# Kernel optimization log

Measured on AMD Instinct MI355X. Metric: run time of the kernel, lower is better.

## Reference

```python
import jax, jax.numpy as jnp
import numpy as np

B, NQ, NK, DQ, DK, DV, H = 4, 512, 512, 512, 512, 512, 128
NEG_INF = -1e20


def setup_inputs() -> dict:
    key = jax.random.key(0)
    ks = jax.random.split(key, 7)
    Q = jax.random.normal(ks[0], (B, NQ, DQ), dtype=jnp.float32)
    K = jax.random.normal(ks[1], (B, NK, DK), dtype=jnp.float32)
    V = jax.random.normal(ks[2], (B, NK, DV), dtype=jnp.float32)
    # learned params (LazyLinear, bias=False): y = x @ W with W[in, out]
    Wq = jax.random.normal(ks[3], (DQ, H), dtype=jnp.float32) / np.sqrt(DQ)
    Wk = jax.random.normal(ks[4], (DK, H), dtype=jnp.float32) / np.sqrt(DK)
    wv = jax.random.normal(ks[5], (H,), dtype=jnp.float32) / np.sqrt(H)
    valid_lens = jax.random.randint(ks[6], (B,), 1, NK + 1).astype(jnp.int64)
    return {"Q": Q, "K": K, "V": V, "Wq": Wq, "Wk": Wk, "wv": wv,
            "valid_lens": valid_lens}


def reference(Q, K, V, Wq, Wk, wv, valid_lens):
    # Project queries and keys to shared hidden size H
    Qp = Q @ Wq                      # (B, NQ, H)
    Kp = K @ Wk                      # (B, NK, H)
    # Additive (Bahdanau) broadcast: (B, NQ, NK, H)
    S = jnp.tanh(Qp[:, :, None, :] + Kp[:, None, :, :])
    # Linear score to scalar: (B, NQ, NK)
    scores = jnp.einsum('bqkh,h->bqk', S, wv)
    # Mask positions k >= valid_lens[b] (1-D valid_lens broadcast over queries)
    kv_idx = jnp.arange(scores.shape[-1])[None, None, :]
    mask = kv_idx < valid_lens[:, None, None]
    scores = jnp.where(mask, scores, NEG_INF)
    W = jax.nn.softmax(scores, axis=-1)  # dropout rate 0.0 -> identity
    return jnp.einsum('bqk,bkv->bqv', W, V)
```

## Files before the change

kernel.cpp:

```cpp
#include <hip/hip_runtime.h>

#define B_   4
#define NQ_  512
#define NK_  512
#define D_   512
#define H_   128

typedef __attribute__((ext_vector_type(8))) short short8;
typedef __attribute__((ext_vector_type(8))) unsigned short ushort8;
typedef __attribute__((ext_vector_type(4))) float f32x4;

__device__ __forceinline__ float fexp2(float x) { return __builtin_amdgcn_exp2f(x); }
__device__ __forceinline__ float frcp(float x)  { return __builtin_amdgcn_rcpf(x); }
__device__ __forceinline__ unsigned short f2bf(float f) {
    unsigned int u = __builtin_bit_cast(unsigned int, f);
    u += 0x7FFFu + ((u >> 16) & 1u);
    return (unsigned short)(u >> 16);
}
__device__ __forceinline__ float bf2f(unsigned short h) {
    return __builtin_bit_cast(float, (unsigned int)h << 16);
}


#define WS_EQK   0
#define WS_WP    524288
#define WS_WBF   524544
#define WS_VT    1048832
#define WS_WTHI  1573120
#define WS_WTLO  1638656

__global__ __launch_bounds__(256) void prep_kernel(
    const float* __restrict__ V, const float* __restrict__ Wq,
    const float* __restrict__ Wk, const float* __restrict__ wv,
    const int* __restrict__ valid_lens,
    float* __restrict__ wp, unsigned short* __restrict__ Vt,
    unsigned short* __restrict__ WThi, unsigned short* __restrict__ WTlo)
{
    __shared__ __align__(16) float smem[64 * 69];
    const int t = threadIdx.x;

    if (blockIdx.x < 256) {
        const int id = blockIdx.x;
        const int kt = id & 7, dt = (id >> 3) & 7, b = id >> 6;
        const int vl = valid_lens[b];

        if (kt * 64 >= ((vl + 127) & ~127)) return;

        if (kt * 64 >= vl) {
            #pragma unroll
            for (int p = 0; p < 4; ++p) {
                const int idx = p * 256 + t;
                const int d  = idx >> 4;
                const int k4 = (idx & 15) * 4;
                ushort4 z; z.x = 0; z.y = 0; z.z = 0; z.w = 0;
                *reinterpret_cast<ushort4*>(
                    Vt + ((size_t)b * D_ + dt * 64 + d) * NK_ + kt * 64 + k4) = z;
            }
            return;
        }

        float (*Vl)[69] = (float(*)[69])smem;

        #pragma unroll
        for (int p = 0; p < 4; ++p) {
            const int idx = p * 256 + t;
            const int r  = idx >> 4;
            const int c4 = (idx & 15) * 4;
            const float4 v = *reinterpret_cast<const float4*>(
                V + ((size_t)b * NK_ + kt * 64 + r) * D_ + dt * 64 + c4);
            Vl[r][c4 + 0] = v.x; Vl[r][c4 + 1] = v.y;
            Vl[r][c4 + 2] = v.z; Vl[r][c4 + 3] = v.w;
        }
        __syncthreads();

        #pragma unroll
        for (int p = 0; p < 4; ++p) {
            const int idx = p * 256 + t;
            const int d  = idx >> 4;
            const int k4 = (idx & 15) * 4;
            ushort4 o;
            o.x = f2bf(Vl[k4 + 0][d]); o.y = f2bf(Vl[k4 + 1][d]);
            o.z = f2bf(Vl[k4 + 2][d]); o.w = f2bf(Vl[k4 + 3][d]);
            *reinterpret_cast<ushort4*>(
                Vt + ((size_t)b * D_ + dt * 64 + d) * NK_ + kt * 64 + k4) = o;
        }
    } else {
        if (blockIdx.x == 256 && t < 64) {
            const float2 w2 = reinterpret_cast<const float2*>(wv)[t];
            const float wn0 = -2.0f * w2.x;
            const float wn1 = -2.0f * w2.y;
            reinterpret_cast<float4*>(wp)[t] =
                make_float4(wn0, wn1, wn0 + wn1, 0.0f);
        }
        const int wid  = blockIdx.x - 256;
        const int mat  = wid >> 4;
        const int tile = wid & 15;
        const int kt   = tile >> 1;
        const int ct   = tile & 1;
        const float* __restrict__ Wm = mat ? Wk : Wq;
        float (*Wl)[69] = (float(*)[69])smem;

        #pragma unroll
        for (int p = 0; p < 4; ++p) {
            const int idx = p * 256 + t;
            const int r  = idx >> 4;
            const int c4 = (idx & 15) * 4;
            const float4 v = *reinterpret_cast<const float4*>(
                Wm + (size_t)(kt * 64 + r) * H_ + ct * 64 + c4);
            Wl[r][c4 + 0] = v.x; Wl[r][c4 + 1] = v.y;
            Wl[r][c4 + 2] = v.z; Wl[r][c4 + 3] = v.w;
        }
        __syncthreads();

        const int c  = t >> 2;
        const int kq = (t & 3) * 16;
        ushort8 ph0, pl0, ph1, pl1;
        #pragma unroll
        for (int j = 0; j < 8; ++j) {
            const float x = Wl[kq + j][c];
            const unsigned short h = f2bf(x);
            ph0[j] = h; pl0[j] = f2bf(x - bf2f(h));
        }
        #pragma unroll
        for (int j = 0; j < 8; ++j) {
            const float x = Wl[kq + 8 + j][c];
            const unsigned short h = f2bf(x);
            ph1[j] = h; pl1[j] = f2bf(x - bf2f(h));
        }
        const size_t off =
            ((size_t)(mat * H_ + ct * 64 + c)) * 512 + kt * 64 + kq;
        *reinterpret_cast<ushort8*>(WThi + off)     = ph0;
        *reinterpret_cast<ushort8*>(WThi + off + 8) = ph1;
        *reinterpret_cast<ushort8*>(WTlo + off)     = pl0;
        *reinterpret_cast<ushort8*>(WTlo + off + 8) = pl1;
    }
}

__global__ __launch_bounds__(512, 2) void proj_kernel(
    const float* __restrict__ Q, const float* __restrict__ K,
    const unsigned short* __restrict__ WThi,
    const unsigned short* __restrict__ WTlo,
    const int* __restrict__ valid_lens,
    float* __restrict__ Eqk)
{
    __shared__ __align__(16) unsigned short Ahi[16][520];
    __shared__ __align__(16) unsigned short Alo[16][520];
    const int t  = threadIdx.x;
    const int r0 = blockIdx.x * 16;
    const bool isQ = r0 < 2048;
    const float* __restrict__ X = isQ ? Q : K;
    const int xr0    = isQ ? r0 : r0 - 2048;
    const int matoff = isQ ? 0 : (H_ * 512);

    if (!isQ) {
        const int kr = xr0 & 511;
        const int bb = xr0 >> 9;
        if (kr >= valid_lens[bb]) return;
    }

    #pragma unroll
    for (int p = 0; p < 4; ++p) {
        const int idx = p * 512 + t;
        const int row = idx >> 7;
        const int kq  = (idx & 127) * 4;
        const float4 v = *reinterpret_cast<const float4*>(
            X + (size_t)(xr0 + row) * D_ + kq);
        ushort4 h, l;
        h.x = f2bf(v.x); l.x = f2bf(v.x - bf2f(h.x));
        h.y = f2bf(v.y); l.y = f2bf(v.y - bf2f(h.y));
        h.z = f2bf(v.z); l.z = f2bf(v.z - bf2f(h.z));
        h.w = f2bf(v.w); l.w = f2bf(v.w - bf2f(h.w));
        *reinterpret_cast<ushort4*>(&Ahi[row][kq]) = h;
        *reinterpret_cast<ushort4*>(&Alo[row][kq]) = l;
    }
    __syncthreads();

    const int wave = __builtin_amdgcn_readfirstlane(t >> 6);
    const int lane = t & 63;
    const int m    = lane & 15;
    const int quad = lane >> 4;

    const unsigned short* __restrict__ Bh =
        WThi + matoff + ((size_t)(wave * 16 + m)) * 512 + quad * 8;
    const unsigned short* __restrict__ Bl =
        WTlo + matoff + ((size_t)(wave * 16 + m)) * 512 + quad * 8;

    f32x4 accA = {0.f, 0.f, 0.f, 0.f};
    f32x4 accB = {0.f, 0.f, 0.f, 0.f};
    #pragma unroll
    for (int ksg = 0; ksg < 16; ++ksg) {
        const int kk = ksg * 32;
        const short8 bh = *reinterpret_cast<const short8*>(Bh + kk);
        const short8 bl = *reinterpret_cast<const short8*>(Bl + kk);
        const short8 ah = *reinterpret_cast<const short8*>(&Ahi[m][kk + quad * 8]);
        const short8 al = *reinterpret_cast<const short8*>(&Alo[m][kk + quad * 8]);
        f32x4& acc = (ksg & 1) ? accB : accA;
        acc = __builtin_amdgcn_mfma_f32_16x16x32_bf16(ah, bh, acc, 0, 0, 0);
        acc = __builtin_amdgcn_mfma_f32_16x16x32_bf16(al, bh, acc, 0, 0, 0);
        acc = __builtin_amdgcn_mfma_f32_16x16x32_bf16(ah, bl, acc, 0, 0, 0);
    }

    const float C2 = 2.88539008177792681472f;
    const int col = wave * 16 + m;
    #pragma unroll
    for (int i = 0; i < 4; ++i) {
        Eqk[(size_t)(r0 + quad * 4 + i) * H_ + col] =
            fexp2(C2 * (accA[i] + accB[i]));
    }
}

__global__ __launch_bounds__(512, 4) void score_softmax_kernel(
    const float* __restrict__ Eqk, const float* __restrict__ wp,
    const int* __restrict__ valid_lens, unsigned short* __restrict__ Wbf)
{
    const int rb   = blockIdx.x;
    const int t    = threadIdx.x;
    const int w    = __builtin_amdgcn_readfirstlane(t >> 6);
    const int lane = t & 63;
    const int rloc = w >> 1;
    const int half = w & 1;
    const int row  = rb * 4 + rloc;
    const int b    = row >> 9;

    __shared__ __align__(16) float4 Ks[2 * 64 * 33];
    __shared__ float redM[4][2], redS[4][2];

    const int vl = valid_lens[b];

    const float4* __restrict__ Q4 =
        reinterpret_cast<const float4*>(Eqk + (size_t)row * H_);
    const float4* __restrict__ wp4 = reinterpret_cast<const float4*>(wp);
    const float4* __restrict__ Kp4 =
        reinterpret_cast<const float4*>(Eqk + (size_t)(2048 + b * NK_) * H_);

    float vals[4];

    for (int c = 0; c < 4; ++c) {
        if (c) __syncthreads();
        #pragma unroll
        for (int p = 0; p < 8; ++p) {
            const int hh = p >> 2;
            if (hh * 256 + c * 64 < vl) {
                const int r  = (p & 3) * 16 + (t >> 5);
                const int h4 = t & 31;
                Ks[(hh * 64 + r) * 33 + h4] =
                    Kp4[(size_t)(hh * 256 + c * 64 + r) * 32 + h4];
            }
        }
        __syncthreads();

        float s = 0.0f;
        if (half * 256 + c * 64 < vl) {
            #pragma unroll 4
            for (int g = 0; g < 32; ++g) {
                const float4 kv = Ks[(half * 64 + lane) * 33 + g];
                const float4 qa = Q4[g];
                const float4 wa = wp4[2 * g];
                const float4 wb = wp4[2 * g + 1];
                const float e0 = qa.x * kv.x;
                const float e1 = qa.y * kv.y;
                const float e2 = qa.z * kv.z;
                const float e3 = qa.w * kv.w;
                const float D01 = 1.0f + fmaf(e0, e1, e0 + e1);
                const float D23 = 1.0f + fmaf(e2, e3, e2 + e3);
                const float n01 = fmaf(wa.y, e0, fmaf(wa.x, e1, wa.z));
                const float n23 = fmaf(wb.y, e2, fmaf(wb.x, e3, wb.z));
                const float N   = fmaf(n23, D01, n01 * D23);
                s = fmaf(N, frcp(D01 * D23), s);
            }
        }
        vals[c] = s;
    }

    const float L2E = 1.44269504088896340736f;
    float m = -1e30f;
    #pragma unroll
    for (int c = 0; c < 4; ++c) {
        const int k = half * 256 + c * 64 + lane;
        vals[c] = (k < vl) ? vals[c] : -1e30f;
        m = fmaxf(m, vals[c]);
    }
    #pragma unroll
    for (int off = 32; off >= 1; off >>= 1)
        m = fmaxf(m, __shfl_xor(m, off, 64));
    float sum = 0.0f;
    #pragma unroll
    for (int c = 0; c < 4; ++c)
        sum += fexp2((vals[c] - m) * L2E);
    #pragma unroll
    for (int off = 32; off >= 1; off >>= 1)
        sum += __shfl_xor(sum, off, 64);

    if (lane == 0) { redM[rloc][half] = m; redS[rloc][half] = sum; }
    __syncthreads();

    const float m0 = redM[rloc][0], m1 = redM[rloc][1];
    const float s0 = redS[rloc][0], s1 = redS[rloc][1];
    const float M  = fmaxf(m0, m1);
    const float S  = fmaf(s0, fexp2((m0 - M) * L2E),
                          s1 * fexp2((m1 - M) * L2E));
    const float inv = frcp(S);

    unsigned short* __restrict__ dst = Wbf + (size_t)row * NK_ + half * 256;
    #pragma unroll
    for (int c = 0; c < 4; ++c)
        dst[c * 64 + lane] = f2bf(fexp2((vals[c] - M) * L2E) * inv);
}

__global__ __launch_bounds__(256) void av_gemm_kernel(
    const unsigned short* __restrict__ Wbf, const unsigned short* __restrict__ Vt,
    const int* __restrict__ valid_lens, float* __restrict__ O)
{
    const int c0 = blockIdx.x * 64;
    const int r0 = blockIdx.y * 64;
    const int b  = blockIdx.z;
    const int t  = threadIdx.x;
    const int wave = __builtin_amdgcn_readfirstlane(t >> 6);
    const int lane = t & 63;
    const int m    = lane & 15;
    const int quad = lane >> 4;

    const int vl = valid_lens[b];

    __shared__ unsigned short Al [64][136];
    __shared__ unsigned short Btl[64][136];

    f32x4 acc0 = {0.f,0.f,0.f,0.f}, acc1 = {0.f,0.f,0.f,0.f};
    f32x4 acc2 = {0.f,0.f,0.f,0.f}, acc3 = {0.f,0.f,0.f,0.f};

    for (int kc = 0; kc < 4; ++kc) {
        if (kc * 128 >= vl) break;
        if (kc) __syncthreads();
        #pragma unroll
        for (int p = 0; p < 4; ++p) {
            const int idx = p * 256 + t;
            const int rl = idx >> 4;
            const int k8 = (idx & 15) * 8;
            *reinterpret_cast<uint4*>(&Al[rl][k8]) =
                *reinterpret_cast<const uint4*>(
                    Wbf + ((size_t)b * NQ_ + r0 + rl) * NK_ + kc * 128 + k8);
            *reinterpret_cast<uint4*>(&Btl[rl][k8]) =
                *reinterpret_cast<const uint4*>(
                    Vt + ((size_t)b * D_ + c0 + rl) * NK_ + kc * 128 + k8);
        }
        __syncthreads();

        #pragma unroll
        for (int sub = 0; sub < 4; ++sub) {
            const int kcol = sub * 32 + quad * 8;
            const short8 a = *reinterpret_cast<const short8*>(&Al[wave * 16 + m][kcol]);
            const short8 b0 = *reinterpret_cast<const short8*>(&Btl[ 0 + m][kcol]);
            const short8 b1 = *reinterpret_cast<const short8*>(&Btl[16 + m][kcol]);
            const short8 b2 = *reinterpret_cast<const short8*>(&Btl[32 + m][kcol]);
            const short8 b3 = *reinterpret_cast<const short8*>(&Btl[48 + m][kcol]);
            acc0 = __builtin_amdgcn_mfma_f32_16x16x32_bf16(a, b0, acc0, 0, 0, 0);
            acc1 = __builtin_amdgcn_mfma_f32_16x16x32_bf16(a, b1, acc1, 0, 0, 0);
            acc2 = __builtin_amdgcn_mfma_f32_16x16x32_bf16(a, b2, acc2, 0, 0, 0);
            acc3 = __builtin_amdgcn_mfma_f32_16x16x32_bf16(a, b3, acc3, 0, 0, 0);
        }
    }

    const size_t rowbase = (size_t)b * NQ_ + r0 + wave * 16 + quad * 4;
    #pragma unroll
    for (int i = 0; i < 4; ++i) {
        float* __restrict__ orow = O + (rowbase + i) * D_ + c0 + m;
        orow[ 0] = acc0[i];
        orow[16] = acc1[i];
        orow[32] = acc2[i];
        orow[48] = acc3[i];
    }
}

extern "C" void kernel_launch(void* const* d_in, const int* in_sizes, int n_in,
                              void* d_out, int out_size, void* d_ws, size_t ws_size,
                              hipStream_t stream) {
    (void)in_sizes; (void)n_in; (void)out_size; (void)ws_size;

    const float* Q   = (const float*)d_in[0];
    const float* K   = (const float*)d_in[1];
    const float* V   = (const float*)d_in[2];
    const float* Wq  = (const float*)d_in[3];
    const float* Wk  = (const float*)d_in[4];
    const float* wv  = (const float*)d_in[5];
    const int*   vl  = (const int*)d_in[6];
    float* out = (float*)d_out;

    float* ws  = (float*)d_ws;
    float* Eqk = ws + WS_EQK;
    float* wp  = ws + WS_WP;
    unsigned short* Wbf  = (unsigned short*)(ws + WS_WBF);
    unsigned short* Vt   = (unsigned short*)(ws + WS_VT);
    unsigned short* WThi = (unsigned short*)(ws + WS_WTHI);
    unsigned short* WTlo = (unsigned short*)(ws + WS_WTLO);

    prep_kernel<<<dim3(288), 256, 0, stream>>>(V, Wq, Wk, wv, vl, wp, Vt, WThi, WTlo);
    proj_kernel<<<dim3(256), 512, 0, stream>>>(Q, K, WThi, WTlo, vl, Eqk);
    score_softmax_kernel<<<dim3(512), 512, 0, stream>>>(Eqk, wp, vl, Wbf);
    av_gemm_kernel<<<dim3(8, 8, 4), 256, 0, stream>>>(Wbf, Vt, vl, out);
}
```

Measured before the change: 115.4 us.

## Fuse prep and projection kernels, split weights on the fly

```diff
diff --git a/kernel.cpp b/kernel.cpp
--- a/kernel.cpp
+++ b/kernel.cpp
@@ -26,21 +26,21 @@
 #define WS_WP    524288
 #define WS_WBF   524544
 #define WS_VT    1048832
-#define WS_WTHI  1573120
-#define WS_WTLO  1638656
-
-__global__ __launch_bounds__(256) void prep_kernel(
-    const float* __restrict__ V, const float* __restrict__ Wq,
-    const float* __restrict__ Wk, const float* __restrict__ wv,
+
+__global__ __launch_bounds__(512, 4) void projvt_kernel(
+    const float* __restrict__ Q, const float* __restrict__ K,
+    const float* __restrict__ Wq, const float* __restrict__ Wk,
+    const float* __restrict__ V, const float* __restrict__ wv,
     const int* __restrict__ valid_lens,
     float* __restrict__ wp, unsigned short* __restrict__ Vt,
-    unsigned short* __restrict__ WThi, unsigned short* __restrict__ WTlo)
+    float* __restrict__ Eqk)
 {
-    __shared__ __align__(16) float smem[64 * 69];
-    const int t = threadIdx.x;
-
-    if (blockIdx.x < 256) {
-        const int id = blockIdx.x;
+    __shared__ __align__(16) unsigned short smem_u[2 * 32 * 520];
+    const int t  = threadIdx.x;
+    const int bx = blockIdx.x;
+
+    if (bx >= 128) {
+        const int id = bx - 128;
         const int kt = id & 7, dt = (id >> 3) & 7, b = id >> 6;
         const int vl = valid_lens[b];
 
@@ -48,8 +48,8 @@
 
         if (kt * 64 >= vl) {
             #pragma unroll
-            for (int p = 0; p < 4; ++p) {
-                const int idx = p * 256 + t;
+            for (int p = 0; p < 2; ++p) {
+                const int idx = p * 512 + t;
                 const int d  = idx >> 4;
                 const int k4 = (idx & 15) * 4;
                 ushort4 z; z.x = 0; z.y = 0; z.z = 0; z.w = 0;
@@ -59,11 +59,11 @@
             return;
         }
 
-        float (*Vl)[69] = (float(*)[69])smem;
-
-        #pragma unroll
-        for (int p = 0; p < 4; ++p) {
-            const int idx = p * 256 + t;
+        float (*Vl)[69] = (float(*)[69])smem_u;
+
+        #pragma unroll
+        for (int p = 0; p < 2; ++p) {
+            const int idx = p * 512 + t;
             const int r  = idx >> 4;
             const int c4 = (idx & 15) * 4;
             const float4 v = *reinterpret_cast<const float4*>(
@@ -74,8 +74,8 @@
         __syncthreads();
 
         #pragma unroll
-        for (int p = 0; p < 4; ++p) {
-            const int idx = p * 256 + t;
+        for (int p = 0; p < 2; ++p) {
+            const int idx = p * 512 + t;
             const int d  = idx >> 4;
             const int k4 = (idx & 15) * 4;
             ushort4 o;
@@ -84,82 +84,33 @@
             *reinterpret_cast<ushort4*>(
                 Vt + ((size_t)b * D_ + dt * 64 + d) * NK_ + kt * 64 + k4) = o;
         }
-    } else {
-        if (blockIdx.x == 256 && t < 64) {
-            const float2 w2 = reinterpret_cast<const float2*>(wv)[t];
-            const float wn0 = -2.0f * w2.x;
-            const float wn1 = -2.0f * w2.y;
-            reinterpret_cast<float4*>(wp)[t] =
-                make_float4(wn0, wn1, wn0 + wn1, 0.0f);
-        }
-        const int wid  = blockIdx.x - 256;
-        const int mat  = wid >> 4;
-        const int tile = wid & 15;
-        const int kt   = tile >> 1;
-        const int ct   = tile & 1;
-        const float* __restrict__ Wm = mat ? Wk : Wq;
-        float (*Wl)[69] = (float(*)[69])smem;
-
-        #pragma unroll
-        for (int p = 0; p < 4; ++p) {
-            const int idx = p * 256 + t;
-            const int r  = idx >> 4;
-            const int c4 = (idx & 15) * 4;
-            const float4 v = *reinterpret_cast<const float4*>(
-                Wm + (size_t)(kt * 64 + r) * H_ + ct * 64 + c4);
-            Wl[r][c4 + 0] = v.x; Wl[r][c4 + 1] = v.y;
-            Wl[r][c4 + 2] = v.z; Wl[r][c4 + 3] = v.w;
-        }
-        __syncthreads();
-
-        const int c  = t >> 2;
-        const int kq = (t & 3) * 16;
-        ushort8 ph0, pl0, ph1, pl1;
-        #pragma unroll
-        for (int j = 0; j < 8; ++j) {
-            const float x = Wl[kq + j][c];
-            const unsigned short h = f2bf(x);
-            ph0[j] = h; pl0[j] = f2bf(x - bf2f(h));
-        }
-        #pragma unroll
-        for (int j = 0; j < 8; ++j) {
-            const float x = Wl[kq + 8 + j][c];
-            const unsigned short h = f2bf(x);
-            ph1[j] = h; pl1[j] = f2bf(x - bf2f(h));
-        }
-        const size_t off =
-            ((size_t)(mat * H_ + ct * 64 + c)) * 512 + kt * 64 + kq;
-        *reinterpret_cast<ushort8*>(WThi + off)     = ph0;
-        *reinterpret_cast<ushort8*>(WThi + off + 8) = ph1;
-        *reinterpret_cast<ushort8*>(WTlo + off)     = pl0;
-        *reinterpret_cast<ushort8*>(WTlo + off + 8) = pl1;
-    }
-}
-
-__global__ __launch_bounds__(512, 2) void proj_kernel(
-    const float* __restrict__ Q, const float* __restrict__ K,
-    const unsigned short* __restrict__ WThi,
-    const unsigned short* __restrict__ WTlo,
-    const int* __restrict__ valid_lens,
-    float* __restrict__ Eqk)
-{
-    __shared__ __align__(16) unsigned short Ahi[16][520];
-    __shared__ __align__(16) unsigned short Alo[16][520];
-    const int t  = threadIdx.x;
-    const int r0 = blockIdx.x * 16;
-    const bool isQ = r0 < 2048;
-    const float* __restrict__ X = isQ ? Q : K;
-    const int xr0    = isQ ? r0 : r0 - 2048;
-    const int matoff = isQ ? 0 : (H_ * 512);
-
+        return;
+    }
+
+    if (bx == 0 && t < 64) {
+        const float2 w2 = reinterpret_cast<const float2*>(wv)[t];
+        const float wn0 = -2.0f * w2.x;
+        const float wn1 = -2.0f * w2.y;
+        reinterpret_cast<float4*>(wp)[t] =
+            make_float4(wn0, wn1, wn0 + wn1, 0.0f);
+    }
+
+    const bool isQ = bx < 64;
+    const int xr0  = isQ ? bx * 32 : (bx - 64) * 32;
     if (!isQ) {
         const int kr = xr0 & 511;
         const int bb = xr0 >> 9;
         if (kr >= valid_lens[bb]) return;
     }
-
-    #pragma unroll
-    for (int p = 0; p < 4; ++p) {
+    const float* __restrict__ X  = isQ ? Q : K;
+    const float* __restrict__ Wm = isQ ? Wq : Wk;
+    const int er0 = isQ ? xr0 : 2048 + xr0;
+
+    unsigned short (*Ahi)[520] = (unsigned short(*)[520])smem_u;
+    unsigned short (*Alo)[520] = (unsigned short(*)[520])(smem_u + 32 * 520);
+
+    #pragma unroll
+    for (int p = 0; p < 8; ++p) {
         const int idx = p * 512 + t;
         const int row = idx >> 7;
         const int kq  = (idx & 127) * 4;
@@ -179,33 +130,47 @@
     const int lane = t & 63;
     const int m    = lane & 15;
     const int quad = lane >> 4;
-
-    const unsigned short* __restrict__ Bh =
-        WThi + matoff + ((size_t)(wave * 16 + m)) * 512 + quad * 8;
-    const unsigned short* __restrict__ Bl =
-        WTlo + matoff + ((size_t)(wave * 16 + m)) * 512 + quad * 8;
-
-    f32x4 accA = {0.f, 0.f, 0.f, 0.f};
-    f32x4 accB = {0.f, 0.f, 0.f, 0.f};
-    #pragma unroll
+    const int col  = wave * 16 + m;
+    const float* __restrict__ Wcol = Wm + col;
+
+    f32x4 a0A = {0.f,0.f,0.f,0.f}, a0B = {0.f,0.f,0.f,0.f};
+    f32x4 a1A = {0.f,0.f,0.f,0.f}, a1B = {0.f,0.f,0.f,0.f};
+
+    #pragma unroll 2
     for (int ksg = 0; ksg < 16; ++ksg) {
-        const int kk = ksg * 32;
-        const short8 bh = *reinterpret_cast<const short8*>(Bh + kk);
-        const short8 bl = *reinterpret_cast<const short8*>(Bl + kk);
-        const short8 ah = *reinterpret_cast<const short8*>(&Ahi[m][kk + quad * 8]);
-        const short8 al = *reinterpret_cast<const short8*>(&Alo[m][kk + quad * 8]);
-        f32x4& acc = (ksg & 1) ? accB : accA;
-        acc = __builtin_amdgcn_mfma_f32_16x16x32_bf16(ah, bh, acc, 0, 0, 0);
-        acc = __builtin_amdgcn_mfma_f32_16x16x32_bf16(al, bh, acc, 0, 0, 0);
-        acc = __builtin_amdgcn_mfma_f32_16x16x32_bf16(ah, bl, acc, 0, 0, 0);
+        const int k0 = ksg * 32 + quad * 8;
+        float wr[8];
+        #pragma unroll
+        for (int j = 0; j < 8; ++j)
+            wr[j] = Wcol[(size_t)(k0 + j) * H_];
+        short8 bh, bl;
+        #pragma unroll
+        for (int j = 0; j < 8; ++j) {
+            const unsigned short h = f2bf(wr[j]);
+            bh[j] = (short)h;
+            bl[j] = (short)f2bf(wr[j] - bf2f(h));
+        }
+        const short8 ah0 = *reinterpret_cast<const short8*>(&Ahi[     m][k0]);
+        const short8 al0 = *reinterpret_cast<const short8*>(&Alo[     m][k0]);
+        const short8 ah1 = *reinterpret_cast<const short8*>(&Ahi[16 + m][k0]);
+        const short8 al1 = *reinterpret_cast<const short8*>(&Alo[16 + m][k0]);
+        f32x4& A0 = (ksg & 1) ? a0B : a0A;
+        f32x4& A1 = (ksg & 1) ? a1B : a1A;
+        A0 = __builtin_amdgcn_mfma_f32_16x16x32_bf16(ah0, bh, A0, 0, 0, 0);
+        A0 = __builtin_amdgcn_mfma_f32_16x16x32_bf16(al0, bh, A0, 0, 0, 0);
+        A0 = __builtin_amdgcn_mfma_f32_16x16x32_bf16(ah0, bl, A0, 0, 0, 0);
+        A1 = __builtin_amdgcn_mfma_f32_16x16x32_bf16(ah1, bh, A1, 0, 0, 0);
+        A1 = __builtin_amdgcn_mfma_f32_16x16x32_bf16(al1, bh, A1, 0, 0, 0);
+        A1 = __builtin_amdgcn_mfma_f32_16x16x32_bf16(ah1, bl, A1, 0, 0, 0);
     }
 
     const float C2 = 2.88539008177792681472f;
-    const int col = wave * 16 + m;
     #pragma unroll
     for (int i = 0; i < 4; ++i) {
-        Eqk[(size_t)(r0 + quad * 4 + i) * H_ + col] =
-            fexp2(C2 * (accA[i] + accB[i]));
+        Eqk[(size_t)(er0 + quad * 4 + i) * H_ + col] =
+            fexp2(C2 * (a0A[i] + a0B[i]));
+        Eqk[(size_t)(er0 + 16 + quad * 4 + i) * H_ + col] =
+            fexp2(C2 * (a1A[i] + a1B[i]));
     }
 }
 
@@ -388,13 +353,11 @@
     float* ws  = (float*)d_ws;
     float* Eqk = ws + WS_EQK;
     float* wp  = ws + WS_WP;
-    unsigned short* Wbf  = (unsigned short*)(ws + WS_WBF);
-    unsigned short* Vt   = (unsigned short*)(ws + WS_VT);
-    unsigned short* WThi = (unsigned short*)(ws + WS_WTHI);
-    unsigned short* WTlo = (unsigned short*)(ws + WS_WTLO);
-
-    prep_kernel<<<dim3(288), 256, 0, stream>>>(V, Wq, Wk, wv, vl, wp, Vt, WThi, WTlo);
-    proj_kernel<<<dim3(256), 512, 0, stream>>>(Q, K, WThi, WTlo, vl, Eqk);
+    unsigned short* Wbf = (unsigned short*)(ws + WS_WBF);
+    unsigned short* Vt  = (unsigned short*)(ws + WS_VT);
+
+    projvt_kernel<<<dim3(384), 512, 0, stream>>>(Q, K, Wq, Wk, V, wv, vl,
+                                                 wp, Vt, Eqk);
     score_softmax_kernel<<<dim3(512), 512, 0, stream>>>(Eqk, wp, vl, Wbf);
     av_gemm_kernel<<<dim3(8, 8, 4), 256, 0, stream>>>(Wbf, Vt, vl, out);
 }
```

Measured after the change: 110.0 us. 4.7% less time.
